# Kernel optimization log

Hardware: AMD Instinct MI355X
Metric: run time of the kernel (lower is better)

Reference implementation:

```python
import jax, jax.numpy as jnp
import numpy as np

N_NODES = 50000
N_EDGES = 1600000
IN_DIM = 128
HEADS = 2
OUT_CH = 32
NEG_SLOPE = 0.2


def setup_inputs() -> dict:
    key = jax.random.key(0)
    k1, k2, k3, k4, k5, k6 = jax.random.split(key, 6)
    x = jax.random.normal(k1, (N_NODES, IN_DIM), dtype=jnp.float32)
    # Glorot-ish scale for weights
    W = jax.random.normal(k2, (IN_DIM, HEADS * OUT_CH), dtype=jnp.float32) * (1.0 / np.sqrt(IN_DIM))
    att_src = jax.random.normal(k3, (HEADS, OUT_CH), dtype=jnp.float32) * (1.0 / np.sqrt(OUT_CH))
    att_dst = jax.random.normal(k4, (HEADS, OUT_CH), dtype=jnp.float32) * (1.0 / np.sqrt(OUT_CH))
    bias = jnp.zeros((HEADS * OUT_CH,), dtype=jnp.float32)
    edge_index = jax.random.randint(k5, (2, N_EDGES), 0, N_NODES, dtype=jnp.int32)
    return {"x": x, "W": W, "att_src": att_src, "att_dst": att_dst,
            "bias": bias, "edge_index": edge_index}


def reference(x, W, att_src, att_dst, bias, edge_index):
    N = x.shape[0]
    # ELU on input features (IntraGraphAttention.forward)
    xf = jax.nn.elu(x)
    # Shared linear projection, per-head view: [N, H, C]
    h = (xf @ W).reshape(N, HEADS, OUT_CH)
    # add_self_loops=True (PyG GATConv default)
    loops = jnp.arange(N, dtype=edge_index.dtype)
    src = jnp.concatenate([edge_index[0], loops])
    dst = jnp.concatenate([edge_index[1], loops])
    # Per-node attention halves: [N, H]
    a_src = jnp.einsum('nhc,hc->nh', h, att_src)
    a_dst = jnp.einsum('nhc,hc->nh', h, att_dst)
    # Per-edge logits with leaky relu: [E, H]
    logits = a_src[src] + a_dst[dst]
    logits = jnp.where(logits >= 0, logits, NEG_SLOPE * logits)
    # Segment softmax over incoming edges of each dst node
    seg_max = jax.ops.segment_max(logits, dst, num_segments=N)
    e = jnp.exp(logits - seg_max[dst])
    denom = jax.ops.segment_sum(e, dst, num_segments=N)
    alpha = e / (denom[dst] + 1e-16)  # [E, H]
    # Weighted scatter-aggregate of source features: [N, H, C]
    msgs = h[src] * alpha[:, :, None]
    out = jax.ops.segment_sum(msgs, dst, num_segments=N)
    # concat=True -> [N, H*C], plus bias
    return out.reshape(N, HEADS * OUT_CH) + bias
```

## Files before the change

kernel.cpp:

```cpp
#include <hip/hip_runtime.h>
#include <hip/hip_bf16.h>

#define NN 50000
#define EE 1600000

__device__ __forceinline__ float bflo(unsigned u) { return __uint_as_float(u << 16); }
__device__ __forceinline__ float bfhi(unsigned u) { return __uint_as_float(u & 0xffff0000u); }

__global__ __launch_bounds__(256) void k_proj(
    const float* __restrict__ x, const float* __restrict__ W,
    const float* __restrict__ att_src, const float* __restrict__ att_dst,
    unsigned* __restrict__ h2u, float* __restrict__ a_src, float* __restrict__ a_dst) {
  __shared__ float Wl[128 * 64];
  __shared__ float xs[32 * 129];
  int tid = threadIdx.x;
  int row0 = blockIdx.x * 32;
  for (int i = tid; i < 128 * 64; i += 256) Wl[i] = W[i];
  for (int i = tid; i < 32 * 128; i += 256) {
    int r = i >> 7, k = i & 127;
    int row = row0 + r;
    float v = (row < NN) ? x[row * 128 + k] : 0.f;
    xs[r * 129 + k] = v > 0.f ? v : (__expf(v) - 1.f);
  }
  __syncthreads();
  int w = tid >> 6, lane = tid & 63;
  int rs = lane >> 5, c = lane & 31;
  int rbase = w * 8 + rs * 4;
  float a0[4] = {0, 0, 0, 0}, a1[4] = {0, 0, 0, 0};
  const float2* W2 = (const float2*)Wl;
#pragma unroll 4
  for (int k = 0; k < 128; ++k) {
    float2 wv = W2[k * 32 + c];
#pragma unroll
    for (int j = 0; j < 4; ++j) {
      float xv = xs[(rbase + j) * 129 + k];
      a0[j] += xv * wv.x;
      a1[j] += xv * wv.y;
    }
  }
  int hh = c >> 4;
  float2 av_s = ((const float2*)att_src)[c];
  float2 av_d = ((const float2*)att_dst)[c];
#pragma unroll
  for (int j = 0; j < 4; ++j) {
    int row = row0 + rbase + j;
    bool ok = row < NN;
    if (ok) {
      unsigned lo = (unsigned)__bfloat16_as_ushort(__float2bfloat16(a0[j]));
      unsigned hi = (unsigned)__bfloat16_as_ushort(__float2bfloat16(a1[j]));
      h2u[row * 32 + c] = lo | (hi << 16);
    }
    float ps = a0[j] * av_s.x + a1[j] * av_s.y;
    float pd = a0[j] * av_d.x + a1[j] * av_d.y;
#pragma unroll
    for (int o = 1; o < 16; o <<= 1) {
      ps += __shfl_xor(ps, o);
      pd += __shfl_xor(pd, o);
    }
    if (ok && (c & 15) == 0) { a_src[row * 2 + hh] = ps; a_dst[row * 2 + hh] = pd; }
  }
}

__global__ __launch_bounds__(256) void k_build(
    const int* __restrict__ src, const int* __restrict__ dst,
    const float2* __restrict__ a_src2, const float2* __restrict__ a_dst2,
    int* __restrict__ head8, int4* __restrict__ edge4) {
  int e = blockIdx.x * 256 + threadIdx.x;
  int s = src[e], d = dst[e];
  float2 as = a_src2[s], ad = a_dst2[d];
  float l0 = as.x + ad.x; l0 = fmaxf(l0, 0.2f * l0);
  float l1 = as.y + ad.y; l1 = fmaxf(l1, 0.2f * l1);
  int old = atomicExch(&head8[d * 8 + (e & 7)], e);
  edge4[e] = make_int4(s, old, __float_as_int(__expf(l0)), __float_as_int(__expf(l1)));
}

__global__ __launch_bounds__(256) void k_agg(
    const unsigned* __restrict__ h2u, const float* __restrict__ a_src,
    const float* __restrict__ a_dst, const int* __restrict__ head8,
    const int4* __restrict__ edge4, const float* __restrict__ bias,
    float* __restrict__ out) {
  int n = blockIdx.x * 4 + (threadIdx.x >> 6);
  int lane = threadIdx.x & 63;
  int c2 = lane & 31;
  int half = lane >> 5;
  int hh = c2 >> 4;

  float denom = 0.f, acc0 = 0.f, acc1 = 0.f;
  if (half == 0) {
    float l0 = a_src[n * 2 + hh] + a_dst[n * 2 + hh];
    l0 = fmaxf(l0, 0.2f * l0);
    float es = __expf(l0);
    unsigned hv = h2u[n * 32 + c2];
    denom = es; acc0 = es * bflo(hv); acc1 = es * bfhi(hv);
  }

  int e0 = head8[n * 8 + half * 4 + 0];
  int e1 = head8[n * 8 + half * 4 + 1];
  int e2 = head8[n * 8 + half * 4 + 2];
  int e3 = head8[n * 8 + half * 4 + 3];
  while (__any(max(max(e0, e1), max(e2, e3)) >= 0)) {
    int4 p0 = edge4[max(e0, 0)];
    int4 p1 = edge4[max(e1, 0)];
    int4 p2 = edge4[max(e2, 0)];
    int4 p3 = edge4[max(e3, 0)];
    unsigned h0 = h2u[p0.x * 32 + c2], h1 = h2u[p1.x * 32 + c2];
    unsigned h2 = h2u[p2.x * 32 + c2], h3 = h2u[p3.x * 32 + c2];
    float x0 = (e0 >= 0) ? __int_as_float(hh ? p0.w : p0.z) : 0.f;
    float x1 = (e1 >= 0) ? __int_as_float(hh ? p1.w : p1.z) : 0.f;
    float x2 = (e2 >= 0) ? __int_as_float(hh ? p2.w : p2.z) : 0.f;
    float x3 = (e3 >= 0) ? __int_as_float(hh ? p3.w : p3.z) : 0.f;
    denom += (x0 + x1) + (x2 + x3);
    acc0 += x0 * bflo(h0) + x1 * bflo(h1) + x2 * bflo(h2) + x3 * bflo(h3);
    acc1 += x0 * bfhi(h0) + x1 * bfhi(h1) + x2 * bfhi(h2) + x3 * bfhi(h3);
    e0 = (e0 >= 0) ? p0.y : -1;
    e1 = (e1 >= 0) ? p1.y : -1;
    e2 = (e2 >= 0) ? p2.y : -1;
    e3 = (e3 >= 0) ? p3.y : -1;
  }
  denom += __shfl_xor(denom, 32);
  acc0  += __shfl_xor(acc0, 32);
  acc1  += __shfl_xor(acc1, 32);
  if (half == 0) {
    float inv = 1.f / (denom + 1e-16f);
    float2 b = ((const float2*)bias)[c2];
    ((float2*)out)[n * 32 + c2] = make_float2(acc0 * inv + b.x, acc1 * inv + b.y);
  }
}

extern "C" void kernel_launch(void* const* d_in, const int* in_sizes, int n_in,
                              void* d_out, int out_size, void* d_ws, size_t ws_size,
                              hipStream_t stream) {
  const float* x       = (const float*)d_in[0];
  const float* W       = (const float*)d_in[1];
  const float* att_src = (const float*)d_in[2];
  const float* att_dst = (const float*)d_in[3];
  const float* bias    = (const float*)d_in[4];
  const int* edge_index = (const int*)d_in[5];
  const int* esrc = edge_index;
  const int* edst = edge_index + EE;

  char* base = (char*)d_ws;
  unsigned* h2u  = (unsigned*)base;
  float* a_src_b = (float*)(base + 6400000);
  float* a_dst_b = (float*)(base + 6800000);
  int*   head8   = (int*)(base + 7200000);
  int4*  edge4   = (int4*)(base + 8800000);

  hipMemsetAsync(head8, 0xFF, 400000 * sizeof(int), stream);
  k_proj<<<(NN + 31) / 32, 256, 0, stream>>>(x, W, att_src, att_dst, h2u,
                                             a_src_b, a_dst_b);
  k_build<<<EE / 256, 256, 0, stream>>>(esrc, edst, (const float2*)a_src_b,
                                        (const float2*)a_dst_b, head8, edge4);
  k_agg<<<NN / 4, 256, 0, stream>>>(h2u, a_src_b, a_dst_b, head8, edge4, bias,
                                    (float*)d_out);
}
```

Baseline: 250.0 us.

## Widen aggregation to 16 edge chains per node and enlarge projection tile

The edge linked lists are split into 16 chains per destination node instead of 8. In the aggregation kernel each quarter-wave walks 4 chains and loads two packed bf16 words per lane, so memory-level parallelism per node doubles and the serial chain depth halves. The projection kernel now computes 64 rows per block with float4 LDS reads of x and 8 rows per thread. This raises register use and the head-array memset size, and adds an extra shuffle reduction step.

```diff
diff --git a/kernel.cpp b/kernel.cpp
--- a/kernel.cpp
+++ b/kernel.cpp
@@ -12,37 +12,39 @@
     const float* __restrict__ att_src, const float* __restrict__ att_dst,
     unsigned* __restrict__ h2u, float* __restrict__ a_src, float* __restrict__ a_dst) {
   __shared__ float Wl[128 * 64];
-  __shared__ float xs[32 * 129];
+  __shared__ float xs[64 * 132];
   int tid = threadIdx.x;
-  int row0 = blockIdx.x * 32;
+  int row0 = blockIdx.x * 64;
   for (int i = tid; i < 128 * 64; i += 256) Wl[i] = W[i];
-  for (int i = tid; i < 32 * 128; i += 256) {
+  for (int i = tid; i < 64 * 128; i += 256) {
     int r = i >> 7, k = i & 127;
     int row = row0 + r;
     float v = (row < NN) ? x[row * 128 + k] : 0.f;
-    xs[r * 129 + k] = v > 0.f ? v : (__expf(v) - 1.f);
+    xs[r * 132 + k] = v > 0.f ? v : (__expf(v) - 1.f);
   }
   __syncthreads();
   int w = tid >> 6, lane = tid & 63;
   int rs = lane >> 5, c = lane & 31;
-  int rbase = w * 8 + rs * 4;
-  float a0[4] = {0, 0, 0, 0}, a1[4] = {0, 0, 0, 0};
+  int rbase = w * 16 + rs * 8;
+  float a0[8] = {0, 0, 0, 0, 0, 0, 0, 0}, a1[8] = {0, 0, 0, 0, 0, 0, 0, 0};
   const float2* W2 = (const float2*)Wl;
-#pragma unroll 4
-  for (int k = 0; k < 128; ++k) {
-    float2 wv = W2[k * 32 + c];
+  for (int k4 = 0; k4 < 128; k4 += 4) {
+    float2 wv0 = W2[(k4 + 0) * 32 + c];
+    float2 wv1 = W2[(k4 + 1) * 32 + c];
+    float2 wv2 = W2[(k4 + 2) * 32 + c];
+    float2 wv3 = W2[(k4 + 3) * 32 + c];
 #pragma unroll
-    for (int j = 0; j < 4; ++j) {
-      float xv = xs[(rbase + j) * 129 + k];
-      a0[j] += xv * wv.x;
-      a1[j] += xv * wv.y;
+    for (int j = 0; j < 8; ++j) {
+      float4 xv = *(const float4*)&xs[(rbase + j) * 132 + k4];
+      a0[j] += xv.x * wv0.x + xv.y * wv1.x + xv.z * wv2.x + xv.w * wv3.x;
+      a1[j] += xv.x * wv0.y + xv.y * wv1.y + xv.z * wv2.y + xv.w * wv3.y;
     }
   }
   int hh = c >> 4;
   float2 av_s = ((const float2*)att_src)[c];
   float2 av_d = ((const float2*)att_dst)[c];
 #pragma unroll
-  for (int j = 0; j < 4; ++j) {
+  for (int j = 0; j < 8; ++j) {
     int row = row0 + rbase + j;
     bool ok = row < NN;
     if (ok) {
@@ -64,66 +66,74 @@
 __global__ __launch_bounds__(256) void k_build(
     const int* __restrict__ src, const int* __restrict__ dst,
     const float2* __restrict__ a_src2, const float2* __restrict__ a_dst2,
-    int* __restrict__ head8, int4* __restrict__ edge4) {
+    int* __restrict__ head16, int4* __restrict__ edge4) {
   int e = blockIdx.x * 256 + threadIdx.x;
   int s = src[e], d = dst[e];
   float2 as = a_src2[s], ad = a_dst2[d];
   float l0 = as.x + ad.x; l0 = fmaxf(l0, 0.2f * l0);
   float l1 = as.y + ad.y; l1 = fmaxf(l1, 0.2f * l1);
-  int old = atomicExch(&head8[d * 8 + (e & 7)], e);
+  int old = atomicExch(&head16[d * 16 + (e & 15)], e);
   edge4[e] = make_int4(s, old, __float_as_int(__expf(l0)), __float_as_int(__expf(l1)));
 }
 
 __global__ __launch_bounds__(256) void k_agg(
     const unsigned* __restrict__ h2u, const float* __restrict__ a_src,
-    const float* __restrict__ a_dst, const int* __restrict__ head8,
+    const float* __restrict__ a_dst, const int* __restrict__ head16,
     const int4* __restrict__ edge4, const float* __restrict__ bias,
     float* __restrict__ out) {
   int n = blockIdx.x * 4 + (threadIdx.x >> 6);
   int lane = threadIdx.x & 63;
-  int c2 = lane & 31;
-  int half = lane >> 5;
-  int hh = c2 >> 4;
+  int c = lane & 15;
+  int q = lane >> 4;
+  int hh = c >> 3;
 
-  float denom = 0.f, acc0 = 0.f, acc1 = 0.f;
-  if (half == 0) {
+  float denom = 0.f, A0 = 0.f, A1 = 0.f, A2 = 0.f, A3 = 0.f;
+  if (q == 0) {
     float l0 = a_src[n * 2 + hh] + a_dst[n * 2 + hh];
     l0 = fmaxf(l0, 0.2f * l0);
     float es = __expf(l0);
-    unsigned hv = h2u[n * 32 + c2];
-    denom = es; acc0 = es * bflo(hv); acc1 = es * bfhi(hv);
+    uint2 hv = *(const uint2*)&h2u[n * 32 + 2 * c];
+    denom = es;
+    A0 = es * bflo(hv.x); A1 = es * bfhi(hv.x);
+    A2 = es * bflo(hv.y); A3 = es * bfhi(hv.y);
   }
 
-  int e0 = head8[n * 8 + half * 4 + 0];
-  int e1 = head8[n * 8 + half * 4 + 1];
-  int e2 = head8[n * 8 + half * 4 + 2];
-  int e3 = head8[n * 8 + half * 4 + 3];
+  int e0 = head16[n * 16 + q * 4 + 0];
+  int e1 = head16[n * 16 + q * 4 + 1];
+  int e2 = head16[n * 16 + q * 4 + 2];
+  int e3 = head16[n * 16 + q * 4 + 3];
   while (__any(max(max(e0, e1), max(e2, e3)) >= 0)) {
     int4 p0 = edge4[max(e0, 0)];
     int4 p1 = edge4[max(e1, 0)];
     int4 p2 = edge4[max(e2, 0)];
     int4 p3 = edge4[max(e3, 0)];
-    unsigned h0 = h2u[p0.x * 32 + c2], h1 = h2u[p1.x * 32 + c2];
-    unsigned h2 = h2u[p2.x * 32 + c2], h3 = h2u[p3.x * 32 + c2];
+    uint2 h0 = *(const uint2*)&h2u[p0.x * 32 + 2 * c];
+    uint2 h1 = *(const uint2*)&h2u[p1.x * 32 + 2 * c];
+    uint2 h2 = *(const uint2*)&h2u[p2.x * 32 + 2 * c];
+    uint2 h3 = *(const uint2*)&h2u[p3.x * 32 + 2 * c];
     float x0 = (e0 >= 0) ? __int_as_float(hh ? p0.w : p0.z) : 0.f;
     float x1 = (e1 >= 0) ? __int_as_float(hh ? p1.w : p1.z) : 0.f;
     float x2 = (e2 >= 0) ? __int_as_float(hh ? p2.w : p2.z) : 0.f;
     float x3 = (e3 >= 0) ? __int_as_float(hh ? p3.w : p3.z) : 0.f;
     denom += (x0 + x1) + (x2 + x3);
-    acc0 += x0 * bflo(h0) + x1 * bflo(h1) + x2 * bflo(h2) + x3 * bflo(h3);
-    acc1 += x0 * bfhi(h0) + x1 * bfhi(h1) + x2 * bfhi(h2) + x3 * bfhi(h3);
+    A0 += x0 * bflo(h0.x) + x1 * bflo(h1.x) + x2 * bflo(h2.x) + x3 * bflo(h3.x);
+    A1 += x0 * bfhi(h0.x) + x1 * bfhi(h1.x) + x2 * bfhi(h2.x) + x3 * bfhi(h3.x);
+    A2 += x0 * bflo(h0.y) + x1 * bflo(h1.y) + x2 * bflo(h2.y) + x3 * bflo(h3.y);
+    A3 += x0 * bfhi(h0.y) + x1 * bfhi(h1.y) + x2 * bfhi(h2.y) + x3 * bfhi(h3.y);
     e0 = (e0 >= 0) ? p0.y : -1;
     e1 = (e1 >= 0) ? p1.y : -1;
     e2 = (e2 >= 0) ? p2.y : -1;
     e3 = (e3 >= 0) ? p3.y : -1;
   }
-  denom += __shfl_xor(denom, 32);
-  acc0  += __shfl_xor(acc0, 32);
-  acc1  += __shfl_xor(acc1, 32);
-  if (half == 0) {
+  denom += __shfl_xor(denom, 16); A0 += __shfl_xor(A0, 16);
+  A1 += __shfl_xor(A1, 16); A2 += __shfl_xor(A2, 16); A3 += __shfl_xor(A3, 16);
+  denom += __shfl_xor(denom, 32); A0 += __shfl_xor(A0, 32);
+  A1 += __shfl_xor(A1, 32); A2 += __shfl_xor(A2, 32); A3 += __shfl_xor(A3, 32);
+  if (q == 0) {
     float inv = 1.f / (denom + 1e-16f);
-    float2 b = ((const float2*)bias)[c2];
-    ((float2*)out)[n * 32 + c2] = make_float2(acc0 * inv + b.x, acc1 * inv + b.y);
+    float4 b = ((const float4*)bias)[c];
+    ((float4*)out)[n * 16 + c] =
+        make_float4(A0 * inv + b.x, A1 * inv + b.y, A2 * inv + b.z, A3 * inv + b.w);
   }
 }
 
@@ -143,14 +153,14 @@
   unsigned* h2u  = (unsigned*)base;
   float* a_src_b = (float*)(base + 6400000);
   float* a_dst_b = (float*)(base + 6800000);
-  int*   head8   = (int*)(base + 7200000);
-  int4*  edge4   = (int4*)(base + 8800000);
+  int*   head16  = (int*)(base + 7200000);
+  int4*  edge4   = (int4*)(base + 10400000);
 
-  hipMemsetAsync(head8, 0xFF, 400000 * sizeof(int), stream);
-  k_proj<<<(NN + 31) / 32, 256, 0, stream>>>(x, W, att_src, att_dst, h2u,
+  hipMemsetAsync(head16, 0xFF, 800000 * sizeof(int), stream);
+  k_proj<<<(NN + 63) / 64, 256, 0, stream>>>(x, W, att_src, att_dst, h2u,
                                              a_src_b, a_dst_b);
   k_build<<<EE / 256, 256, 0, stream>>>(esrc, edst, (const float2*)a_src_b,
-                                        (const float2*)a_dst_b, head8, edge4);
-  k_agg<<<NN / 4, 256, 0, stream>>>(h2u, a_src_b, a_dst_b, head8, edge4, bias,
+                                        (const float2*)a_dst_b, head16, edge4);
+  k_agg<<<NN / 4, 256, 0, stream>>>(h2u, a_src_b, a_dst_b, head16, edge4, bias,
                                     (float*)d_out);
 }
```

New measurement: 262.3 us. 4.9% more time.

## Split projection into MFMA bf16 GEMM and fused attention-logit pre-kernel

Applied to the files above, without the earlier changes.

Attention logits are now computed by a separate kernel that folds att_src/att_dst into W (W·att per head) and reduces ELU(x) against those 128x2 vectors per node; the same kernel also initializes head8, replacing the memset. The feature projection moves to a bf16 MFMA 16x16x32 kernel with bf16-converted W and x tiles held in LDS. The aim is to replace the scalar FP32 FMA GEMM with matrix cores and remove a launch, at the cost of reading x twice and computing logits from fp32 values while h is stored in bf16.

```diff
diff --git a/kernel.cpp b/kernel.cpp
--- a/kernel.cpp
+++ b/kernel.cpp
@@ -4,60 +4,100 @@
 #define NN 50000
 #define EE 1600000
 
+using short8 = __attribute__((ext_vector_type(8))) short;
+using float4v = __attribute__((ext_vector_type(4))) float;
+
 __device__ __forceinline__ float bflo(unsigned u) { return __uint_as_float(u << 16); }
 __device__ __forceinline__ float bfhi(unsigned u) { return __uint_as_float(u & 0xffff0000u); }
+__device__ __forceinline__ unsigned short f2bf(float v) {
+  return __bfloat16_as_ushort(__float2bfloat16(v));
+}
 
-__global__ __launch_bounds__(256) void k_proj(
+__global__ __launch_bounds__(256) void k_pre(
     const float* __restrict__ x, const float* __restrict__ W,
     const float* __restrict__ att_src, const float* __restrict__ att_dst,
-    unsigned* __restrict__ h2u, float* __restrict__ a_src, float* __restrict__ a_dst) {
-  __shared__ float Wl[128 * 64];
-  __shared__ float xs[32 * 129];
+    float2* __restrict__ a_src2, float2* __restrict__ a_dst2,
+    int* __restrict__ head8, int nblocks) {
+  __shared__ float wa_s[128][2], wa_d[128][2];
   int tid = threadIdx.x;
-  int row0 = blockIdx.x * 32;
-  for (int i = tid; i < 128 * 64; i += 256) Wl[i] = W[i];
-  for (int i = tid; i < 32 * 128; i += 256) {
-    int r = i >> 7, k = i & 127;
+  {
+    int k = tid >> 1, hh = tid & 1;
+    const float* wrow = W + k * 64 + hh * 32;
+    const float* as = att_src + hh * 32;
+    const float* ad = att_dst + hh * 32;
+    float ss = 0.f, dd = 0.f;
+#pragma unroll 8
+    for (int c = 0; c < 32; ++c) { float wv = wrow[c]; ss += wv * as[c]; dd += wv * ad[c]; }
+    wa_s[k][hh] = ss; wa_d[k][hh] = dd;
+  }
+  int gsize = nblocks * 256;
+  for (int i = blockIdx.x * 256 + tid; i < NN * 8; i += gsize) head8[i] = -1;
+  __syncthreads();
+  int w = tid >> 6, lane = tid & 63;
+  int nwaves = nblocks * 4;
+  for (int n = blockIdx.x * 4 + w; n < NN; n += nwaves) {
+    float x0 = x[n * 128 + lane], x1 = x[n * 128 + 64 + lane];
+    x0 = x0 > 0.f ? x0 : __expf(x0) - 1.f;
+    x1 = x1 > 0.f ? x1 : __expf(x1) - 1.f;
+    float s0 = x0 * wa_s[lane][0] + x1 * wa_s[lane + 64][0];
+    float s1 = x0 * wa_s[lane][1] + x1 * wa_s[lane + 64][1];
+    float d0 = x0 * wa_d[lane][0] + x1 * wa_d[lane + 64][0];
+    float d1 = x0 * wa_d[lane][1] + x1 * wa_d[lane + 64][1];
+#pragma unroll
+    for (int o = 32; o > 0; o >>= 1) {
+      s0 += __shfl_xor(s0, o); s1 += __shfl_xor(s1, o);
+      d0 += __shfl_xor(d0, o); d1 += __shfl_xor(d1, o);
+    }
+    if (lane == 0) { a_src2[n] = make_float2(s0, s1); a_dst2[n] = make_float2(d0, d1); }
+  }
+}
+
+__global__ __launch_bounds__(256) void k_projm(
+    const float* __restrict__ x, const float* __restrict__ W,
+    unsigned* __restrict__ h2u) {
+  __shared__ unsigned short Wt[64 * 136];
+  __shared__ unsigned short xs[64 * 136];
+  int tid = threadIdx.x;
+  int row0 = blockIdx.x * 64;
+  for (int i = tid; i < 8192; i += 256) {
+    int k = i >> 6, n = i & 63;
+    Wt[n * 136 + k] = f2bf(W[i]);
+  }
+  for (int i = tid; i < 4096; i += 256) {
+    int r = i >> 6, k2 = (i & 63) * 2;
     int row = row0 + r;
-    float v = (row < NN) ? x[row * 128 + k] : 0.f;
-    xs[r * 129 + k] = v > 0.f ? v : (__expf(v) - 1.f);
+    float v0 = 0.f, v1 = 0.f;
+    if (row < NN) { float2 xv = *(const float2*)&x[row * 128 + k2]; v0 = xv.x; v1 = xv.y; }
+    v0 = v0 > 0.f ? v0 : __expf(v0) - 1.f;
+    v1 = v1 > 0.f ? v1 : __expf(v1) - 1.f;
+    *(unsigned*)&xs[r * 136 + k2] = (unsigned)f2bf(v0) | ((unsigned)f2bf(v1) << 16);
   }
   __syncthreads();
   int w = tid >> 6, lane = tid & 63;
-  int rs = lane >> 5, c = lane & 31;
-  int rbase = w * 8 + rs * 4;
-  float a0[4] = {0, 0, 0, 0}, a1[4] = {0, 0, 0, 0};
-  const float2* W2 = (const float2*)Wl;
-#pragma unroll 4
-  for (int k = 0; k < 128; ++k) {
-    float2 wv = W2[k * 32 + c];
+  int m = lane & 15, quad = lane >> 4;
+  float4v acc[4] = {{0,0,0,0},{0,0,0,0},{0,0,0,0},{0,0,0,0}};
 #pragma unroll
-    for (int j = 0; j < 4; ++j) {
-      float xv = xs[(rbase + j) * 129 + k];
-      a0[j] += xv * wv.x;
-      a1[j] += xv * wv.y;
+  for (int ks = 0; ks < 4; ++ks) {
+    int koff = quad * 8 + ks * 32;
+    short8 af = *(const short8*)&xs[(w * 16 + m) * 136 + koff];
+#pragma unroll
+    for (int nt = 0; nt < 4; ++nt) {
+      short8 bf = *(const short8*)&Wt[(nt * 16 + m) * 136 + koff];
+      acc[nt] = __builtin_amdgcn_mfma_f32_16x16x32_bf16(af, bf, acc[nt], 0, 0, 0);
     }
   }
-  int hh = c >> 4;
-  float2 av_s = ((const float2*)att_src)[c];
-  float2 av_d = ((const float2*)att_dst)[c];
 #pragma unroll
-  for (int j = 0; j < 4; ++j) {
-    int row = row0 + rbase + j;
-    bool ok = row < NN;
-    if (ok) {
-      unsigned lo = (unsigned)__bfloat16_as_ushort(__float2bfloat16(a0[j]));
-      unsigned hi = (unsigned)__bfloat16_as_ushort(__float2bfloat16(a1[j]));
-      h2u[row * 32 + c] = lo | (hi << 16);
+  for (int nt = 0; nt < 4; ++nt) {
+#pragma unroll
+    for (int reg = 0; reg < 4; ++reg) {
+      float v = acc[nt][reg];
+      float vhi = __shfl_xor(v, 1);
+      int row = row0 + w * 16 + quad * 4 + reg;
+      if (!(m & 1) && row < NN) {
+        h2u[row * 32 + nt * 8 + (m >> 1)] =
+            (unsigned)f2bf(v) | ((unsigned)f2bf(vhi) << 16);
+      }
     }
-    float ps = a0[j] * av_s.x + a1[j] * av_s.y;
-    float pd = a0[j] * av_d.x + a1[j] * av_d.y;
-#pragma unroll
-    for (int o = 1; o < 16; o <<= 1) {
-      ps += __shfl_xor(ps, o);
-      pd += __shfl_xor(pd, o);
-    }
-    if (ok && (c & 15) == 0) { a_src[row * 2 + hh] = ps; a_dst[row * 2 + hh] = pd; }
   }
 }
 
@@ -75,8 +115,8 @@
 }
 
 __global__ __launch_bounds__(256) void k_agg(
-    const unsigned* __restrict__ h2u, const float* __restrict__ a_src,
-    const float* __restrict__ a_dst, const int* __restrict__ head8,
+    const unsigned* __restrict__ h2u, const float2* __restrict__ a_src2,
+    const float2* __restrict__ a_dst2, const int4* __restrict__ head8v,
     const int4* __restrict__ edge4, const float* __restrict__ bias,
     float* __restrict__ out) {
   int n = blockIdx.x * 4 + (threadIdx.x >> 6);
@@ -87,17 +127,16 @@
 
   float denom = 0.f, acc0 = 0.f, acc1 = 0.f;
   if (half == 0) {
-    float l0 = a_src[n * 2 + hh] + a_dst[n * 2 + hh];
+    float2 as = a_src2[n], ad = a_dst2[n];
+    float l0 = (hh ? as.y + ad.y : as.x + ad.x);
     l0 = fmaxf(l0, 0.2f * l0);
     float es = __expf(l0);
     unsigned hv = h2u[n * 32 + c2];
     denom = es; acc0 = es * bflo(hv); acc1 = es * bfhi(hv);
   }
 
-  int e0 = head8[n * 8 + half * 4 + 0];
-  int e1 = head8[n * 8 + half * 4 + 1];
-  int e2 = head8[n * 8 + half * 4 + 2];
-  int e3 = head8[n * 8 + half * 4 + 3];
+  int4 hd = head8v[n * 2 + half];
+  int e0 = hd.x, e1 = hd.y, e2 = hd.z, e3 = hd.w;
   while (__any(max(max(e0, e1), max(e2, e3)) >= 0)) {
     int4 p0 = edge4[max(e0, 0)];
     int4 p1 = edge4[max(e1, 0)];
@@ -141,16 +180,16 @@
 
   char* base = (char*)d_ws;
   unsigned* h2u  = (unsigned*)base;
-  float* a_src_b = (float*)(base + 6400000);
-  float* a_dst_b = (float*)(base + 6800000);
-  int*   head8   = (int*)(base + 7200000);
-  int4*  edge4   = (int4*)(base + 8800000);
+  float2* a_src2 = (float2*)(base + 6400000);
+  float2* a_dst2 = (float2*)(base + 6800000);
+  int*    head8  = (int*)(base + 7200000);
+  int4*   edge4  = (int4*)(base + 8800000);
 
-  hipMemsetAsync(head8, 0xFF, 400000 * sizeof(int), stream);
-  k_proj<<<(NN + 31) / 32, 256, 0, stream>>>(x, W, att_src, att_dst, h2u,
-                                             a_src_b, a_dst_b);
-  k_build<<<EE / 256, 256, 0, stream>>>(esrc, edst, (const float2*)a_src_b,
-                                        (const float2*)a_dst_b, head8, edge4);
-  k_agg<<<NN / 4, 256, 0, stream>>>(h2u, a_src_b, a_dst_b, head8, edge4, bias,
-                                    (float*)d_out);
+  const int PRE_BLOCKS = 1024;
+  k_pre<<<PRE_BLOCKS, 256, 0, stream>>>(x, W, att_src, att_dst, a_src2, a_dst2,
+                                        head8, PRE_BLOCKS);
+  k_projm<<<(NN + 63) / 64, 256, 0, stream>>>(x, W, h2u);
+  k_build<<<EE / 256, 256, 0, stream>>>(esrc, edst, a_src2, a_dst2, head8, edge4);
+  k_agg<<<NN / 4, 256, 0, stream>>>(h2u, a_src2, a_dst2, (const int4*)head8,
+                                    edge4, bias, (float*)d_out);
 }
```

New measurement: 248.3 us. Within noise of the previous version (-0.7%).
